# Kernel tuning notes

Hardware: AMD Instinct MI355X
Metric: run time of the kernel (lower is better)

The kernel has to match this reference:

```python
import jax, jax.numpy as jnp
import numpy as np

N = 100000
NFEAT = 128
NHID = 16
HEADS = 8
NCLASS = 40
E = 1600000
NEG_SLOPE = 0.2  # PyG GATConv default


def glorot(key, shape):
    fan = shape[0] + shape[-1]
    limit = float(np.sqrt(6.0 / fan))
    return jax.random.uniform(key, shape, jnp.float32, -limit, limit)


def setup_inputs() -> dict:
    key = jax.random.key(0)
    ks = jax.random.split(key, 10)
    x = jax.random.normal(ks[0], (N, NFEAT), jnp.float32)
    adj = jnp.zeros((1,), jnp.float32)  # unused by forward, kept for signature parity
    edge_index = jax.random.randint(ks[1], (2, E), 0, N, jnp.int64)
    # layer 1: GATConv(NFEAT, NHID, heads=HEADS)
    W1 = glorot(ks[2], (NFEAT, HEADS * NHID))
    att_src1 = glorot(ks[3], (HEADS, NHID))
    att_dst1 = glorot(ks[4], (HEADS, NHID))
    b1 = jnp.zeros((HEADS * NHID,), jnp.float32)
    # layer 2: GATConv(HEADS*NHID, NCLASS, heads=1)
    W2 = glorot(ks[5], (HEADS * NHID, NCLASS))
    att_src2 = glorot(ks[6], (1, NCLASS))
    att_dst2 = glorot(ks[7], (1, NCLASS))
    b2 = jnp.zeros((NCLASS,), jnp.float32)
    return {"x": x, "adj": adj, "edge_index": edge_index,
            "W1": W1, "att_src1": att_src1, "att_dst1": att_dst1, "b1": b1,
            "W2": W2, "att_src2": att_src2, "att_dst2": att_dst2, "b2": b2}


def gat_conv(x, W, att_src, att_dst, bias, src, dst, heads, out_ch):
    n = x.shape[0]
    h = (x @ W).reshape(n, heads, out_ch)              # [N,H,C]
    a_src = (h * att_src[None]).sum(-1)                # [N,H]
    a_dst = (h * att_dst[None]).sum(-1)                # [N,H]
    e = jax.nn.leaky_relu(a_src[src] + a_dst[dst], NEG_SLOPE)  # [E,H]
    # softmax over incoming edges of each destination node
    m = jax.ops.segment_max(e, dst, num_segments=n)
    e = jnp.exp(e - m[dst])
    s = jax.ops.segment_sum(e, dst, num_segments=n)
    alpha = e / s[dst]                                  # [E,H]
    msg = h[src] * alpha[:, :, None]                    # [E,H,C]
    out = jax.ops.segment_sum(msg, dst, num_segments=n)  # [N,H,C]
    return out.reshape(n, heads * out_ch) + bias


def reference(x, adj, edge_index, W1, att_src1, att_dst1, b1, W2, att_src2, att_dst2, b2):
    # PyG GATConv adds self-loops by default
    loops = jnp.arange(N, dtype=edge_index.dtype)
    src = jnp.concatenate([edge_index[0], loops])
    dst = jnp.concatenate([edge_index[1], loops])
    # eval mode: F.dropout is identity
    h = jax.nn.elu(gat_conv(x, W1, att_src1, att_dst1, b1, src, dst, HEADS, NHID))
    h = jax.nn.elu(gat_conv(h, W2, att_src2, att_dst2, b2, src, dst, 1, NCLASS))
    return jax.nn.log_softmax(h, axis=1)
```

## Files before the change

kernel.cpp:

```cpp
#include <hip/hip_runtime.h>
#include <stdint.h>

#define NEG_SLOPE 0.2f

__device__ __forceinline__ float lrelu(float v) { return v >= 0.f ? v : NEG_SLOPE * v; }
__device__ __forceinline__ float elu(float v) { return v > 0.f ? v : expm1f(v); }
__device__ __forceinline__ float pexp(float v) { return __expf(lrelu(v)); }

typedef _Float16 h16x2 __attribute__((ext_vector_type(2)));
typedef _Float16 half8 __attribute__((ext_vector_type(8)));
typedef float floatx4 __attribute__((ext_vector_type(4)));

__device__ __forceinline__ void fma_h2(float& a0, float& a1, float p, unsigned u) {
    h16x2 h = __builtin_bit_cast(h16x2, u);
    a0 += p * (float)h[0];
    a1 += p * (float)h[1];
}


__global__ void zero_deg_kernel(int* __restrict__ deg, int n) {
    int t = blockIdx.x * blockDim.x + threadIdx.x;
    if (t < n) deg[t] = 0;
}

__global__ void hist_kernel(const int* __restrict__ ei, int* __restrict__ deg,
                            int* __restrict__ rank, int E, int n) {
    int e = blockIdx.x * blockDim.x + threadIdx.x;
    if (e >= E) return;
    int s = ei[e], d = ei[E + e];
    int r = -1;
    if ((unsigned)s < (unsigned)n && (unsigned)d < (unsigned)n)
        r = atomicAdd(&deg[d], 1);
    rank[e] = r;
}

#define SCAN_T 256
#define SCAN_TILE 1024

__global__ __launch_bounds__(SCAN_T) void scan_p1_kernel(const int* __restrict__ deg,
                                                         int* __restrict__ bsum, int n) {
    __shared__ int red[SCAN_T];
    int t = threadIdx.x;
    int base = blockIdx.x * SCAN_TILE + t * 4;
    int s = 0;
    #pragma unroll
    for (int i = 0; i < 4; i++) {
        int idx = base + i;
        if (idx < n) s += deg[idx];
    }
    red[t] = s;
    __syncthreads();
    for (int off = SCAN_T / 2; off; off >>= 1) {
        if (t < off) red[t] += red[t + off];
        __syncthreads();
    }
    if (t == 0) bsum[blockIdx.x] = red[0];
}

__global__ __launch_bounds__(1024) void scan_p2_kernel(int* __restrict__ bsum, int nb,
                                                       int* __restrict__ total) {
    __shared__ int sh[1024];
    int t = threadIdx.x;
    int v = (t < nb) ? bsum[t] : 0;
    sh[t] = v;
    __syncthreads();
    for (int off = 1; off < 1024; off <<= 1) {
        int add = (t >= off) ? sh[t - off] : 0;
        __syncthreads();
        sh[t] += add;
        __syncthreads();
    }
    if (t < nb) bsum[t] = sh[t] - v;
    if (t == nb - 1) *total = sh[t];
}

__global__ __launch_bounds__(SCAN_T) void scan_p3_kernel(const int* __restrict__ deg,
                                                         const int* __restrict__ bsum,
                                                         int* __restrict__ row_ptr, int n) {
    __shared__ int red[SCAN_T];
    int t = threadIdx.x;
    int base = blockIdx.x * SCAN_TILE + t * 4;
    int v[4];
    int s = 0;
    #pragma unroll
    for (int i = 0; i < 4; i++) {
        int idx = base + i;
        v[i] = (idx < n) ? deg[idx] : 0;
        s += v[i];
    }
    red[t] = s;
    __syncthreads();
    for (int off = 1; off < SCAN_T; off <<= 1) {
        int add = (t >= off) ? red[t - off] : 0;
        __syncthreads();
        red[t] += add;
        __syncthreads();
    }
    int excl = red[t] - s + bsum[blockIdx.x];
    #pragma unroll
    for (int i = 0; i < 4; i++) {
        int idx = base + i;
        if (idx < n) row_ptr[idx] = excl;
        excl += v[i];
    }
}

__global__ void scatter_kernel(const int* __restrict__ ei, const int* __restrict__ rank,
                               const int* __restrict__ row_ptr,
                               int* __restrict__ csr_src, int E, int n) {
    int e = blockIdx.x * blockDim.x + threadIdx.x;
    if (e >= E) return;
    int r = rank[e];
    if (r < 0) return;
    int s = ei[e], d = ei[E + e];
    csr_src[row_ptr[d] + r] = s;
}


__global__ void w1t_kernel(const float* __restrict__ W1, _Float16* __restrict__ w1t) {
    int t = blockIdx.x * 256 + threadIdx.x;
    int col = t >> 7, k = t & 127;
    w1t[col * 128 + k] = (_Float16)W1[k * 128 + col];
}

__global__ void w2t_kernel(const float* __restrict__ W2, _Float16* __restrict__ w2t) {
    int t = blockIdx.x * 256 + threadIdx.x;
    if (t >= 48 * 128) return;
    int col = t >> 7, k = t & 127;
    w2t[t] = (col < 40) ? (_Float16)W2[k * 40 + col] : (_Float16)0.f;
}


__global__ __launch_bounds__(256) void gemm1_mfma_kernel(
    const float* __restrict__ x, const _Float16* __restrict__ w1t,
    const float* __restrict__ as1, const float* __restrict__ ad1,
    _Float16* __restrict__ h1h, float* __restrict__ a1s, float* __restrict__ a1d, int n) {
    __shared__ __align__(16) char Wl[32768];
    const int tid = threadIdx.x;
    {
        const uint4* Wg = (const uint4*)w1t;
        #pragma unroll
        for (int i = 0; i < 8; i++) {
            int it = tid + i * 256;
            uint4 v = Wg[it];
            int b = it * 16;
            *(uint4*)&Wl[b ^ (((b >> 8) & 7) << 4)] = v;
        }
    }
    const int wave = tid >> 6, lane = tid & 63;
    const int cl = lane & 15, g = lane >> 4;
    const int wbase = blockIdx.x * 64 + wave * 16;

    int arow = wbase + cl;
    if (arow >= n) arow = n - 1;
    half8 afr[4];
    #pragma unroll
    for (int t = 0; t < 4; t++) {
        const float4 v0 = *(const float4*)&x[(size_t)arow * 128 + 32 * t + g * 8];
        const float4 v1 = *(const float4*)&x[(size_t)arow * 128 + 32 * t + g * 8 + 4];
        afr[t][0] = (_Float16)v0.x; afr[t][1] = (_Float16)v0.y;
        afr[t][2] = (_Float16)v0.z; afr[t][3] = (_Float16)v0.w;
        afr[t][4] = (_Float16)v1.x; afr[t][5] = (_Float16)v1.y;
        afr[t][6] = (_Float16)v1.z; afr[t][7] = (_Float16)v1.w;
    }
    __syncthreads();

    #pragma unroll
    for (int ct = 0; ct < 8; ct++) {
        const int col = ct * 16 + cl;
        half8 bfr[4];
        #pragma unroll
        for (int t = 0; t < 4; t++) {
            int b = (col << 8) + 64 * t + 16 * g;
            bfr[t] = *(half8*)&Wl[b ^ ((col & 7) << 4)];
        }
        floatx4 acc = {0.f, 0.f, 0.f, 0.f};
        #pragma unroll
        for (int t = 0; t < 4; t++)
            acc = __builtin_amdgcn_mfma_f32_16x16x32_f16(afr[t], bfr[t], acc, 0, 0, 0);
        const float av = as1[col], dv = ad1[col];
        #pragma unroll
        for (int i = 0; i < 4; i++) {
            int r = wbase + g * 4 + i;
            float hv = acc[i];
            if (r < n) h1h[(size_t)r * 128 + col] = (_Float16)hv;
            float ps = hv * av, pd = hv * dv;
            ps += __shfl_xor(ps, 1); ps += __shfl_xor(ps, 2);
            ps += __shfl_xor(ps, 4); ps += __shfl_xor(ps, 8);
            pd += __shfl_xor(pd, 1); pd += __shfl_xor(pd, 2);
            pd += __shfl_xor(pd, 4); pd += __shfl_xor(pd, 8);
            if (cl == 0 && r < n) {
                a1s[r * 8 + ct] = ps;
                a1d[r * 8 + ct] = pd;
            }
        }
    }
}

__global__ __launch_bounds__(256) void agg1_kernel(const int* __restrict__ row_ptr,
                                                   const int* __restrict__ csr_src,
                                                   const float* __restrict__ a1s,
                                                   const float* __restrict__ a1d,
                                                   const uint4* __restrict__ h1q,
                                                   const float* __restrict__ b1,
                                                   _Float16* __restrict__ h2h, int n) {
    int lane = threadIdx.x & 63;
    int d = blockIdx.x * 4 + (threadIdx.x >> 6);
    if (d >= n) return;
    const int g = lane >> 4;
    const int q = lane & 15;
    const int h = q >> 1;
    const float adh = a1d[d * 8 + h];

    float acc[8];
    #pragma unroll
    for (int i = 0; i < 8; i++) acc[i] = 0.f;
    float sum = 0.f;
    if (g == 0) {
        uint4 w = h1q[(size_t)d * 16 + q];
        float ps = pexp(a1s[d * 8 + h] + adh);
        fma_h2(acc[0], acc[1], ps, w.x);
        fma_h2(acc[2], acc[3], ps, w.y);
        fma_h2(acc[4], acc[5], ps, w.z);
        fma_h2(acc[6], acc[7], ps, w.w);
        sum = ps;
    }
    int beg = row_ptr[d], end = row_ptr[d + 1];
    int e = beg + g;
    for (; e + 4 < end; e += 8) {
        int s0 = csr_src[e], s1 = csr_src[e + 4];
        uint4 w0 = h1q[(size_t)s0 * 16 + q];
        uint4 w1 = h1q[(size_t)s1 * 16 + q];
        float p0 = pexp(a1s[s0 * 8 + h] + adh);
        float p1 = pexp(a1s[s1 * 8 + h] + adh);
        fma_h2(acc[0], acc[1], p0, w0.x);
        fma_h2(acc[2], acc[3], p0, w0.y);
        fma_h2(acc[4], acc[5], p0, w0.z);
        fma_h2(acc[6], acc[7], p0, w0.w);
        fma_h2(acc[0], acc[1], p1, w1.x);
        fma_h2(acc[2], acc[3], p1, w1.y);
        fma_h2(acc[4], acc[5], p1, w1.z);
        fma_h2(acc[6], acc[7], p1, w1.w);
        sum += p0 + p1;
    }
    for (; e < end; e += 4) {
        int s = csr_src[e];
        uint4 w = h1q[(size_t)s * 16 + q];
        float p = pexp(a1s[s * 8 + h] + adh);
        fma_h2(acc[0], acc[1], p, w.x);
        fma_h2(acc[2], acc[3], p, w.y);
        fma_h2(acc[4], acc[5], p, w.z);
        fma_h2(acc[6], acc[7], p, w.w);
        sum += p;
    }
    sum += __shfl_xor(sum, 16); sum += __shfl_xor(sum, 32);
    #pragma unroll
    for (int i = 0; i < 8; i++) {
        acc[i] += __shfl_xor(acc[i], 16);
        acc[i] += __shfl_xor(acc[i], 32);
    }
    if (g == 0) {
        float rs = 1.f / sum;
        float4 b0 = *(const float4*)&b1[8 * q];
        float4 b4 = *(const float4*)&b1[8 * q + 4];
        half8 o;
        o[0] = (_Float16)elu(acc[0] * rs + b0.x);
        o[1] = (_Float16)elu(acc[1] * rs + b0.y);
        o[2] = (_Float16)elu(acc[2] * rs + b0.z);
        o[3] = (_Float16)elu(acc[3] * rs + b0.w);
        o[4] = (_Float16)elu(acc[4] * rs + b4.x);
        o[5] = (_Float16)elu(acc[5] * rs + b4.y);
        o[6] = (_Float16)elu(acc[6] * rs + b4.z);
        o[7] = (_Float16)elu(acc[7] * rs + b4.w);
        *(half8*)&h2h[(size_t)d * 128 + 8 * q] = o;
    }
}


__global__ __launch_bounds__(256) void gemm2_mfma_kernel(
    const _Float16* __restrict__ h2h, const _Float16* __restrict__ w2t,
    const float* __restrict__ as2, const float* __restrict__ ad2,
    float* __restrict__ h3f, _Float16* __restrict__ h3h,
    float* __restrict__ a2s, float* __restrict__ a2d, int n) {
    const int tid = threadIdx.x;
    const int wave = tid >> 6, lane = tid & 63;
    const int cl = lane & 15, g = lane >> 4;
    const int wbase = blockIdx.x * 64 + wave * 16;

    int arow = wbase + cl;
    if (arow >= n) arow = n - 1;
    half8 afr[4];
    #pragma unroll
    for (int t = 0; t < 4; t++)
        afr[t] = *(const half8*)&h2h[(size_t)arow * 128 + 32 * t + 8 * g];

    float ps[4] = {0.f, 0.f, 0.f, 0.f};
    float pd[4] = {0.f, 0.f, 0.f, 0.f};
    #pragma unroll
    for (int ct = 0; ct < 3; ct++) {
        const int col = ct * 16 + cl;
        half8 bfr[4];
        #pragma unroll
        for (int t = 0; t < 4; t++)
            bfr[t] = *(const half8*)&w2t[col * 128 + 32 * t + 8 * g];
        floatx4 acc = {0.f, 0.f, 0.f, 0.f};
        #pragma unroll
        for (int t = 0; t < 4; t++)
            acc = __builtin_amdgcn_mfma_f32_16x16x32_f16(afr[t], bfr[t], acc, 0, 0, 0);
        const bool cv = (col < 40);
        const float av = cv ? as2[col] : 0.f;
        const float dv = cv ? ad2[col] : 0.f;
        #pragma unroll
        for (int i = 0; i < 4; i++) {
            int r = wbase + g * 4 + i;
            float hv = acc[i];
            if (cv && r < n) {
                h3f[(size_t)r * 40 + col] = hv;
                h3h[(size_t)r * 40 + col] = (_Float16)hv;
            }
            ps[i] += hv * av;
            pd[i] += hv * dv;
        }
    }
    #pragma unroll
    for (int i = 0; i < 4; i++) {
        float s = ps[i], dd = pd[i];
        s += __shfl_xor(s, 1); s += __shfl_xor(s, 2);
        s += __shfl_xor(s, 4); s += __shfl_xor(s, 8);
        dd += __shfl_xor(dd, 1); dd += __shfl_xor(dd, 2);
        dd += __shfl_xor(dd, 4); dd += __shfl_xor(dd, 8);
        int r = wbase + g * 4 + i;
        if (cl == 0 && r < n) {
            a2s[r] = s;
            a2d[r] = dd;
        }
    }
}

__global__ __launch_bounds__(256) void agg2_final_kernel(const int* __restrict__ row_ptr,
                                                         const int* __restrict__ csr_src,
                                                         const float* __restrict__ a2s,
                                                         const float* __restrict__ a2d,
                                                         const float* __restrict__ h3f,
                                                         const unsigned* __restrict__ h3p,
                                                         const float* __restrict__ b2,
                                                         float* __restrict__ out, int n) {
    int lane = threadIdx.x & 63;
    int d = blockIdx.x * 4 + (threadIdx.x >> 6);
    if (d >= n) return;
    const int g = lane >> 5;
    const int q = lane & 31;
    const bool act = (q < 20);

    float2 hv = make_float2(0.f, 0.f);
    if (act && g == 0) hv = *(const float2*)&h3f[(size_t)d * 40 + 2 * q];
    const float adh = a2d[d];

    float acc0 = 0.f, acc1 = 0.f, sum = 0.f;
    if (g == 0) {
        float ps = pexp(a2s[d] + adh);
        acc0 = ps * hv.x; acc1 = ps * hv.y; sum = ps;
    }
    int beg = row_ptr[d], end = row_ptr[d + 1];
    int e = beg + g;
    for (; e + 6 < end; e += 8) {
        int s0 = csr_src[e],     s1 = csr_src[e + 2];
        int s2 = csr_src[e + 4], s3 = csr_src[e + 6];
        float a0 = a2s[s0], a1 = a2s[s1], a2 = a2s[s2], a3 = a2s[s3];
        unsigned w0 = 0u, w1 = 0u, w2 = 0u, w3 = 0u;
        if (act) {
            w0 = h3p[(size_t)s0 * 20 + q]; w1 = h3p[(size_t)s1 * 20 + q];
            w2 = h3p[(size_t)s2 * 20 + q]; w3 = h3p[(size_t)s3 * 20 + q];
        }
        float p0 = pexp(a0 + adh), p1 = pexp(a1 + adh);
        float p2 = pexp(a2 + adh), p3 = pexp(a3 + adh);
        fma_h2(acc0, acc1, p0, w0);
        fma_h2(acc0, acc1, p1, w1);
        fma_h2(acc0, acc1, p2, w2);
        fma_h2(acc0, acc1, p3, w3);
        sum += (p0 + p1) + (p2 + p3);
    }
    for (; e < end; e += 2) {
        int s = csr_src[e];
        float pe = pexp(a2s[s] + adh);
        unsigned w = act ? h3p[(size_t)s * 20 + q] : 0u;
        fma_h2(acc0, acc1, pe, w);
        sum += pe;
    }
    sum += __shfl_xor(sum, 32);
    acc0 += __shfl_xor(acc0, 32);
    acc1 += __shfl_xor(acc1, 32);

    float rs = 1.f / sum;
    float v0 = -3.0e38f, v1 = -3.0e38f;
    if (act) {
        v0 = elu(acc0 * rs + b2[2 * q]);
        v1 = elu(acc1 * rs + b2[2 * q + 1]);
    }
    float mx = (act && g == 0) ? fmaxf(v0, v1) : -3.0e38f;
    #pragma unroll
    for (int off = 32; off; off >>= 1) mx = fmaxf(mx, __shfl_xor(mx, off, 64));
    float es = (act && g == 0) ? (__expf(v0 - mx) + __expf(v1 - mx)) : 0.f;
    #pragma unroll
    for (int off = 32; off; off >>= 1) es += __shfl_xor(es, off, 64);
    if (act && g == 0) {
        float ls = logf(es);
        float2 o;
        o.x = v0 - mx - ls;
        o.y = v1 - mx - ls;
        *(float2*)&out[(size_t)d * 40 + 2 * q] = o;
    }
}

extern "C" void kernel_launch(void* const* d_in, const int* in_sizes, int n_in,
                              void* d_out, int out_size, void* d_ws, size_t ws_size,
                              hipStream_t stream) {
    const float* x   = (const float*)d_in[0];
    const int*   ei  = (const int*)d_in[2];
    const float* W1  = (const float*)d_in[3];
    const float* as1 = (const float*)d_in[4];
    const float* ad1 = (const float*)d_in[5];
    const float* b1  = (const float*)d_in[6];
    const float* W2  = (const float*)d_in[7];
    const float* as2 = (const float*)d_in[8];
    const float* ad2 = (const float*)d_in[9];
    const float* b2  = (const float*)d_in[10];
    float* out = (float*)d_out;

    const int n = in_sizes[0] / 128;
    const int E = in_sizes[2] / 2;
    const int nb = (n + SCAN_TILE - 1) / SCAN_TILE;

    float* ws = (float*)d_ws;
    _Float16* h1h = (_Float16*)ws;
    _Float16* h2h = (_Float16*)(ws + (size_t)n * 64);
    float* A  = ws + (size_t)n * 128;
    int* deg    = (int*)A;
    int* bsum   = deg + n;
    float* a1s  = A;
    float* a1d  = A + (size_t)n * 8;
    float* a2s  = A;
    float* a2d  = A + (size_t)n;
    int* row_ptr = (int*)(A + (size_t)n * 16);
    int* csr_src = row_ptr + (n + 1);
    int* rank    = csr_src + E;
    _Float16* w1t = (_Float16*)(((uintptr_t)(rank + E) + 63) & ~(uintptr_t)63);
    _Float16* w2t = w1t + 128 * 128;
    _Float16* h3h = h1h;
    float* h3f = ws + (size_t)n * 20;

    w1t_kernel<<<64, 256, 0, stream>>>(W1, w1t);
    w2t_kernel<<<24, 256, 0, stream>>>(W2, w2t);
    zero_deg_kernel<<<(n + 255) / 256, 256, 0, stream>>>(deg, n);
    hist_kernel<<<(E + 255) / 256, 256, 0, stream>>>(ei, deg, rank, E, n);
    scan_p1_kernel<<<nb, SCAN_T, 0, stream>>>(deg, bsum, n);
    scan_p2_kernel<<<1, 1024, 0, stream>>>(bsum, nb, &row_ptr[n]);
    scan_p3_kernel<<<nb, SCAN_T, 0, stream>>>(deg, bsum, row_ptr, n);
    scatter_kernel<<<(E + 255) / 256, 256, 0, stream>>>(ei, rank, row_ptr, csr_src, E, n);

    gemm1_mfma_kernel<<<(n + 63) / 64, 256, 0, stream>>>(x, w1t, as1, ad1, h1h, a1s, a1d, n);
    agg1_kernel<<<(n + 3) / 4, 256, 0, stream>>>(row_ptr, csr_src, a1s, a1d,
                                                 (const uint4*)h1h, b1, h2h, n);

    gemm2_mfma_kernel<<<(n + 63) / 64, 256, 0, stream>>>(h2h, w2t, as2, ad2,
                                                         h3f, h3h, a2s, a2d, n);
    agg2_final_kernel<<<(n + 3) / 4, 256, 0, stream>>>(row_ptr, csr_src, a2s, a2d, h3f,
                                                       (const unsigned*)h3h, b2, out, n);
}
```

Measured before the change: 419.3 us.

## Pack layer-2 features with source scores and fuse prep kernels

Layer-2 features are now stored as one padded 128-byte row per node, holding the fp16 features together with the source attention score. A gather therefore fetches the score and the features from the same cache line, and the separate fp32 copy of the features is no longer written. The weight-transpose and degree-zeroing kernels are merged into one launch, the layer-1 aggregation loop gets a 4-way unrolled main loop for more loads in flight, and the source-index check moves from the histogram to the scatter kernel. In exchange the padding makes each node's row larger, and the self-loop term now uses fp16 features instead of fp32.

```diff
diff --git a/kernel.cpp b/kernel.cpp
--- a/kernel.cpp
+++ b/kernel.cpp
@@ -18,19 +18,29 @@
 }
 
 
-__global__ void zero_deg_kernel(int* __restrict__ deg, int n) {
-    int t = blockIdx.x * blockDim.x + threadIdx.x;
+__global__ void prep_kernel(const float* __restrict__ W1, const float* __restrict__ W2,
+                            _Float16* __restrict__ w1t, _Float16* __restrict__ w2t,
+                            int* __restrict__ deg, int n) {
+    int t = blockIdx.x * 256 + threadIdx.x;
     if (t < n) deg[t] = 0;
-}
+    if (t < 128 * 128) {
+        int col = t >> 7, k = t & 127;
+        w1t[col * 128 + k] = (_Float16)W1[k * 128 + col];
+    }
+    if (t < 48 * 128) {
+        int col = t >> 7, k = t & 127;
+        w2t[t] = (col < 40) ? (_Float16)W2[k * 40 + col] : (_Float16)0.f;
+    }
+}
+
 
 __global__ void hist_kernel(const int* __restrict__ ei, int* __restrict__ deg,
                             int* __restrict__ rank, int E, int n) {
     int e = blockIdx.x * blockDim.x + threadIdx.x;
     if (e >= E) return;
-    int s = ei[e], d = ei[E + e];
+    int d = ei[E + e];
     int r = -1;
-    if ((unsigned)s < (unsigned)n && (unsigned)d < (unsigned)n)
-        r = atomicAdd(&deg[d], 1);
+    if ((unsigned)d < (unsigned)n) r = atomicAdd(&deg[d], 1);
     rank[e] = r;
 }
 
@@ -113,21 +123,8 @@
     int r = rank[e];
     if (r < 0) return;
     int s = ei[e], d = ei[E + e];
+    if ((unsigned)s >= (unsigned)n) return;
     csr_src[row_ptr[d] + r] = s;
-}
-
-
-__global__ void w1t_kernel(const float* __restrict__ W1, _Float16* __restrict__ w1t) {
-    int t = blockIdx.x * 256 + threadIdx.x;
-    int col = t >> 7, k = t & 127;
-    w1t[col * 128 + k] = (_Float16)W1[k * 128 + col];
-}
-
-__global__ void w2t_kernel(const float* __restrict__ W2, _Float16* __restrict__ w2t) {
-    int t = blockIdx.x * 256 + threadIdx.x;
-    if (t >= 48 * 128) return;
-    int col = t >> 7, k = t & 127;
-    w2t[t] = (col < 40) ? (_Float16)W2[k * 40 + col] : (_Float16)0.f;
 }
 
 
@@ -227,20 +224,37 @@
     }
     int beg = row_ptr[d], end = row_ptr[d + 1];
     int e = beg + g;
+    for (; e + 12 < end; e += 16) {
+        int s0 = csr_src[e],     s1 = csr_src[e + 4];
+        int s2 = csr_src[e + 8], s3 = csr_src[e + 12];
+        uint4 w0 = h1q[(size_t)s0 * 16 + q];
+        uint4 w1 = h1q[(size_t)s1 * 16 + q];
+        uint4 w2 = h1q[(size_t)s2 * 16 + q];
+        uint4 w3 = h1q[(size_t)s3 * 16 + q];
+        float p0 = pexp(a1s[s0 * 8 + h] + adh);
+        float p1 = pexp(a1s[s1 * 8 + h] + adh);
+        float p2 = pexp(a1s[s2 * 8 + h] + adh);
+        float p3 = pexp(a1s[s3 * 8 + h] + adh);
+        fma_h2(acc[0], acc[1], p0, w0.x); fma_h2(acc[2], acc[3], p0, w0.y);
+        fma_h2(acc[4], acc[5], p0, w0.z); fma_h2(acc[6], acc[7], p0, w0.w);
+        fma_h2(acc[0], acc[1], p1, w1.x); fma_h2(acc[2], acc[3], p1, w1.y);
+        fma_h2(acc[4], acc[5], p1, w1.z); fma_h2(acc[6], acc[7], p1, w1.w);
+        fma_h2(acc[0], acc[1], p2, w2.x); fma_h2(acc[2], acc[3], p2, w2.y);
+        fma_h2(acc[4], acc[5], p2, w2.z); fma_h2(acc[6], acc[7], p2, w2.w);
+        fma_h2(acc[0], acc[1], p3, w3.x); fma_h2(acc[2], acc[3], p3, w3.y);
+        fma_h2(acc[4], acc[5], p3, w3.z); fma_h2(acc[6], acc[7], p3, w3.w);
+        sum += (p0 + p1) + (p2 + p3);
+    }
     for (; e + 4 < end; e += 8) {
         int s0 = csr_src[e], s1 = csr_src[e + 4];
         uint4 w0 = h1q[(size_t)s0 * 16 + q];
         uint4 w1 = h1q[(size_t)s1 * 16 + q];
         float p0 = pexp(a1s[s0 * 8 + h] + adh);
         float p1 = pexp(a1s[s1 * 8 + h] + adh);
-        fma_h2(acc[0], acc[1], p0, w0.x);
-        fma_h2(acc[2], acc[3], p0, w0.y);
-        fma_h2(acc[4], acc[5], p0, w0.z);
-        fma_h2(acc[6], acc[7], p0, w0.w);
-        fma_h2(acc[0], acc[1], p1, w1.x);
-        fma_h2(acc[2], acc[3], p1, w1.y);
-        fma_h2(acc[4], acc[5], p1, w1.z);
-        fma_h2(acc[6], acc[7], p1, w1.w);
+        fma_h2(acc[0], acc[1], p0, w0.x); fma_h2(acc[2], acc[3], p0, w0.y);
+        fma_h2(acc[4], acc[5], p0, w0.z); fma_h2(acc[6], acc[7], p0, w0.w);
+        fma_h2(acc[0], acc[1], p1, w1.x); fma_h2(acc[2], acc[3], p1, w1.y);
+        fma_h2(acc[4], acc[5], p1, w1.z); fma_h2(acc[6], acc[7], p1, w1.w);
         sum += p0 + p1;
     }
     for (; e < end; e += 4) {
@@ -280,8 +294,7 @@
 __global__ __launch_bounds__(256) void gemm2_mfma_kernel(
     const _Float16* __restrict__ h2h, const _Float16* __restrict__ w2t,
     const float* __restrict__ as2, const float* __restrict__ ad2,
-    float* __restrict__ h3f, _Float16* __restrict__ h3h,
-    float* __restrict__ a2s, float* __restrict__ a2d, int n) {
+    _Float16* __restrict__ h3pk, float* __restrict__ a2d, int n) {
     const int tid = threadIdx.x;
     const int wave = tid >> 6, lane = tid & 63;
     const int cl = lane & 15, g = lane >> 4;
@@ -314,10 +327,8 @@
         for (int i = 0; i < 4; i++) {
             int r = wbase + g * 4 + i;
             float hv = acc[i];
-            if (cv && r < n) {
-                h3f[(size_t)r * 40 + col] = hv;
-                h3h[(size_t)r * 40 + col] = (_Float16)hv;
-            }
+            if (cv && r < n)
+                h3pk[(size_t)r * 64 + 2 + col] = (_Float16)hv;
             ps[i] += hv * av;
             pd[i] += hv * dv;
         }
@@ -331,7 +342,7 @@
         dd += __shfl_xor(dd, 4); dd += __shfl_xor(dd, 8);
         int r = wbase + g * 4 + i;
         if (cl == 0 && r < n) {
-            a2s[r] = s;
+            ((float*)h3pk)[(size_t)r * 32] = s;
             a2d[r] = dd;
         }
     }
@@ -339,38 +350,38 @@
 
 __global__ __launch_bounds__(256) void agg2_final_kernel(const int* __restrict__ row_ptr,
                                                          const int* __restrict__ csr_src,
-                                                         const float* __restrict__ a2s,
+                                                         const unsigned* __restrict__ h3u,
                                                          const float* __restrict__ a2d,
-                                                         const float* __restrict__ h3f,
-                                                         const unsigned* __restrict__ h3p,
                                                          const float* __restrict__ b2,
                                                          float* __restrict__ out, int n) {
+    const float* h3a = (const float*)h3u;
     int lane = threadIdx.x & 63;
     int d = blockIdx.x * 4 + (threadIdx.x >> 6);
     if (d >= n) return;
     const int g = lane >> 5;
     const int q = lane & 31;
     const bool act = (q < 20);
-
-    float2 hv = make_float2(0.f, 0.f);
-    if (act && g == 0) hv = *(const float2*)&h3f[(size_t)d * 40 + 2 * q];
     const float adh = a2d[d];
+
+    h16x2 hsel = {(_Float16)0.f, (_Float16)0.f};
+    if (act && g == 0) hsel = __builtin_bit_cast(h16x2, h3u[(size_t)d * 32 + 1 + q]);
 
     float acc0 = 0.f, acc1 = 0.f, sum = 0.f;
     if (g == 0) {
-        float ps = pexp(a2s[d] + adh);
-        acc0 = ps * hv.x; acc1 = ps * hv.y; sum = ps;
+        float ps = pexp(h3a[(size_t)d * 32] + adh);
+        acc0 = ps * (float)hsel[0]; acc1 = ps * (float)hsel[1]; sum = ps;
     }
     int beg = row_ptr[d], end = row_ptr[d + 1];
     int e = beg + g;
     for (; e + 6 < end; e += 8) {
         int s0 = csr_src[e],     s1 = csr_src[e + 2];
         int s2 = csr_src[e + 4], s3 = csr_src[e + 6];
-        float a0 = a2s[s0], a1 = a2s[s1], a2 = a2s[s2], a3 = a2s[s3];
+        float a0 = h3a[(size_t)s0 * 32], a1 = h3a[(size_t)s1 * 32];
+        float a2 = h3a[(size_t)s2 * 32], a3 = h3a[(size_t)s3 * 32];
         unsigned w0 = 0u, w1 = 0u, w2 = 0u, w3 = 0u;
         if (act) {
-            w0 = h3p[(size_t)s0 * 20 + q]; w1 = h3p[(size_t)s1 * 20 + q];
-            w2 = h3p[(size_t)s2 * 20 + q]; w3 = h3p[(size_t)s3 * 20 + q];
+            w0 = h3u[(size_t)s0 * 32 + 1 + q]; w1 = h3u[(size_t)s1 * 32 + 1 + q];
+            w2 = h3u[(size_t)s2 * 32 + 1 + q]; w3 = h3u[(size_t)s3 * 32 + 1 + q];
         }
         float p0 = pexp(a0 + adh), p1 = pexp(a1 + adh);
         float p2 = pexp(a2 + adh), p3 = pexp(a3 + adh);
@@ -382,8 +393,8 @@
     }
     for (; e < end; e += 2) {
         int s = csr_src[e];
-        float pe = pexp(a2s[s] + adh);
-        unsigned w = act ? h3p[(size_t)s * 20 + q] : 0u;
+        float pe = pexp(h3a[(size_t)s * 32] + adh);
+        unsigned w = act ? h3u[(size_t)s * 32 + 1 + q] : 0u;
         fma_h2(acc0, acc1, pe, w);
         sum += pe;
     }
@@ -437,21 +448,17 @@
     float* A  = ws + (size_t)n * 128;
     int* deg    = (int*)A;
     int* bsum   = deg + n;
-    float* a1s  = A;
-    float* a1d  = A + (size_t)n * 8;
-    float* a2s  = A;
-    float* a2d  = A + (size_t)n;
+    float* a1s = A;
+    float* a1d = A + (size_t)n * 8;
+    float* a2d = A;
     int* row_ptr = (int*)(A + (size_t)n * 16);
     int* csr_src = row_ptr + (n + 1);
     int* rank    = csr_src + E;
     _Float16* w1t = (_Float16*)(((uintptr_t)(rank + E) + 63) & ~(uintptr_t)63);
     _Float16* w2t = w1t + 128 * 128;
-    _Float16* h3h = h1h;
-    float* h3f = ws + (size_t)n * 20;
-
-    w1t_kernel<<<64, 256, 0, stream>>>(W1, w1t);
-    w2t_kernel<<<24, 256, 0, stream>>>(W2, w2t);
-    zero_deg_kernel<<<(n + 255) / 256, 256, 0, stream>>>(deg, n);
+    _Float16* h3pk = h1h;
+
+    prep_kernel<<<(n + 255) / 256, 256, 0, stream>>>(W1, W2, w1t, w2t, deg, n);
     hist_kernel<<<(E + 255) / 256, 256, 0, stream>>>(ei, deg, rank, E, n);
     scan_p1_kernel<<<nb, SCAN_T, 0, stream>>>(deg, bsum, n);
     scan_p2_kernel<<<1, 1024, 0, stream>>>(bsum, nb, &row_ptr[n]);
@@ -462,8 +469,7 @@
     agg1_kernel<<<(n + 3) / 4, 256, 0, stream>>>(row_ptr, csr_src, a1s, a1d,
                                                  (const uint4*)h1h, b1, h2h, n);
 
-    gemm2_mfma_kernel<<<(n + 63) / 64, 256, 0, stream>>>(h2h, w2t, as2, ad2,
-                                                         h3f, h3h, a2s, a2d, n);
-    agg2_final_kernel<<<(n + 3) / 4, 256, 0, stream>>>(row_ptr, csr_src, a2s, a2d, h3f,
-                                                       (const unsigned*)h3h, b2, out, n);
-}
+    gemm2_mfma_kernel<<<(n + 63) / 64, 256, 0, stream>>>(h2h, w2t, as2, ad2, h3pk, a2d, n);
+    agg2_final_kernel<<<(n + 3) / 4, 256, 0, stream>>>(row_ptr, csr_src, (const unsigned*)h3pk,
+                                                       a2d, b2, out, n);
+}
```

Measured after the change: 417.5 us. Within noise of the previous version (-0.4%).
